# Performance work log

Hardware: AMD Instinct MI355X
Metric: run time of the kernel (lower is better)

## Reference

```python
import jax, jax.numpy as jnp
import numpy as np

N, D, H, E, K = 4096, 512, 2048, 8, 2  # tokens, input/output dim, expert hidden, num_experts, top_k


def setup_inputs() -> dict:
    key = jax.random.key(0)
    k_x, k_r, k_w1, k_b1, k_w2, k_b2 = jax.random.split(key, 6)
    input_batch = jax.random.normal(k_x, (N, D), dtype=jnp.float32)
    # Router-style top-k selection: guarantees the K expert ids per token are distinct
    # (required by the torch nonzero-based dispatch) and probabilities are a softmax
    # over the selected logits, matching a standard MoE sampler.
    router_logits = jax.random.normal(k_r, (N, E), dtype=jnp.float32)
    top_vals, top_idx = jax.lax.top_k(router_logits, K)
    probabilities = jax.nn.softmax(top_vals, axis=-1)            # [N, K]
    indices = top_idx.astype(jnp.int64)                          # [N, K]
    scale = 0.02
    W1 = scale * jax.random.normal(k_w1, (E, D, H), dtype=jnp.float32)
    b1 = jnp.zeros((E, H), dtype=jnp.float32)
    W2 = scale * jax.random.normal(k_w2, (E, H, D), dtype=jnp.float32)
    b2 = jnp.zeros((E, D), dtype=jnp.float32)
    return {"input_batch": input_batch, "probabilities": probabilities, "indices": indices,
            "W1": W1, "b1": b1, "W2": W2, "b2": b2}


def reference(input_batch, probabilities, indices, W1, b1, W2, b2):
    # Each expert is a dense 2-layer GELU MLP. The torch module gathers the tokens
    # assigned to each expert, runs the expert, concatenates, sorts back to original
    # flattened [N*K] order, applies probability weighting AFTER the experts, then
    # reshapes to [N, K, D] and sums over K. That is mathematically:
    #   out[t] = sum_k probabilities[t, k] * expert_{indices[t, k]}(input_batch[t])
    h = jax.nn.gelu(jnp.einsum('nd,edh->enh', input_batch, W1) + b1[:, None, :])  # [E, N, H]
    y = jnp.einsum('enh,ehd->end', h, W2) + b2[:, None, :]                         # [E, N, D]
    y = jnp.transpose(y, (1, 0, 2))                                                # [N, E, D]
    sel = jnp.take_along_axis(y, indices[:, :, None], axis=1)                      # [N, K, D]
    output = jnp.sum(sel * probabilities[:, :, None], axis=1)                      # [N, D]
    total_loss = jnp.float32(0.0)  # no sampler / expert aux losses in this config
    return output, total_loss
```

## Files before the change

### kernel.cpp

```cpp
#include <hip/hip_runtime.h>
#include <cstdint>
#include <cstddef>

#define NTOK 4096
#define DIMD 512
#define HIDH 2048
#define NEXP 8
#define TOPK 2
#define NSLOT (NTOK*TOPK)
#define SLACK 128
#define YROWS (NSLOT+SLACK)

#define BM 128
#define BN 128
#define BK 32

typedef short bf16x8_t __attribute__((ext_vector_type(8)));
typedef float f32x4_t  __attribute__((ext_vector_type(4)));

__device__ __forceinline__ unsigned short f2b(float f){
  unsigned int x = __float_as_uint(f);
  unsigned int r = (x + 0x7FFFu + ((x >> 16) & 1u)) >> 16;
  return (unsigned short)r;
}

__device__ __forceinline__ float gelu_tanh(float x) {
  float z2 = 1.5957691216057308f * fmaf(0.044715f * x, x * x, x);
  return x / (1.f + __expf(-z2));
}

__device__ __forceinline__ void gl_lds16(const void* g, void* l){
  __builtin_amdgcn_global_load_lds((const __attribute__((address_space(1))) void*)g,
                                   (__attribute__((address_space(3))) void*)l, 16, 0, 0);
}


__global__ __launch_bounds__(256) void cvt_x(const float* __restrict__ x, unsigned short* __restrict__ xb){
  int i = blockIdx.x*256 + threadIdx.x;
  if (i >= (NTOK*DIMD)/4) return;
  float4 v = ((const float4*)x)[i];
  ushort4 o; o.x=f2b(v.x); o.y=f2b(v.y); o.z=f2b(v.z); o.w=f2b(v.w);
  ((ushort4*)xb)[i] = o;
}

__global__ __launch_bounds__(256) void transpose_cvt(const float* __restrict__ src,
                                                     unsigned short* __restrict__ dst,
                                                     int R, int C){
  int e = blockIdx.z;
  src += (size_t)e*R*C; dst += (size_t)e*R*C;
  int c0 = blockIdx.x*64, r0 = blockIdx.y*64;
  __shared__ float t[64][65];
  int tr = threadIdx.x >> 4, tc = threadIdx.x & 15;
  #pragma unroll
  for (int i=0;i<4;i++){
    int r = tr + i*16;
    float4 v = *(const float4*)(src + (size_t)(r0 + r)*C + c0 + tc*4);
    t[r][tc*4+0]=v.x; t[r][tc*4+1]=v.y; t[r][tc*4+2]=v.z; t[r][tc*4+3]=v.w;
  }
  __syncthreads();
  #pragma unroll
  for (int i=0;i<4;i++){
    int c = tr + i*16;
    ushort4 o;
    o.x = f2b(t[tc*4+0][c]); o.y = f2b(t[tc*4+1][c]);
    o.z = f2b(t[tc*4+2][c]); o.w = f2b(t[tc*4+3][c]);
    *(ushort4*)(dst + (size_t)(c0 + c)*R + r0 + tc*4) = o;
  }
}


__global__ void count_k(const int* __restrict__ I, int* __restrict__ meta){
  int i = blockIdx.x*256+threadIdx.x;
  if (i < NSLOT) atomicAdd(&meta[I[i]], 1);
}
__global__ void scan_k(int* __restrict__ meta){
  if (threadIdx.x==0 && blockIdx.x==0){
    int s=0;
    for(int e=0;e<NEXP;e++){ meta[16+e]=s; s+=meta[e]; }
  }
}
__global__ void fill_k(const int* __restrict__ I, int* __restrict__ meta,
                       int* __restrict__ tokOf, int* __restrict__ rowOf){
  int i = blockIdx.x*256+threadIdx.x;
  if (i < NSLOT){
    int e = I[i];
    int pos = meta[16+e] + atomicAdd(&meta[8+e], 1);
    tokOf[pos] = i >> 1;
    rowOf[i] = pos;
  }
}


__global__ __launch_bounds__(256,2) void gemm1(
    const unsigned short* __restrict__ Xb, const unsigned short* __restrict__ W1t,
    const float* __restrict__ B1, const int* __restrict__ meta,
    const int* __restrict__ tokOf, unsigned short* __restrict__ H)
{
  const int e = blockIdx.z;
  const int cnt = meta[e];
  const int row0 = blockIdx.y * BM;
  if (row0 >= cnt) return;
  const int off = meta[16+e];
  const int h0 = blockIdx.x * BN;

  __shared__ unsigned short As[3][BM*BK];
  __shared__ unsigned short Bs[3][BN*BK];

  const int tid = threadIdx.x;
  const int ar0 = tid >> 2;
  const int ksw = (((tid & 3) ^ ((tid >> 3) & 3)) << 3);
  int s0 = min(off + row0 + ar0,      NSLOT-1);
  int s1 = min(off + row0 + ar0 + 64, NSLOT-1);
  const unsigned short* srcA0 = Xb + (size_t)tokOf[s0]*DIMD + ksw;
  const unsigned short* srcA1 = Xb + (size_t)tokOf[s1]*DIMD + ksw;
  const unsigned short* srcB0 = W1t + ((size_t)e*HIDH + h0 + ar0)*DIMD + ksw;
  const unsigned short* srcB1 = srcB0 + (size_t)64*DIMD;

  const int lane = tid & 63;
  const int wid  = tid >> 6;
  const int wr = (wid >> 1) * 64, wc = (wid & 1) * 64;
  const int l15 = lane & 15, kg = lane >> 4;

  int offA[4], offB[4];
  #pragma unroll
  for (int m=0;m<4;m++){
    int r  = wr + m*16 + l15;
    int rb = wc + m*16 + l15;
    offA[m] = r *BK + ((kg ^ ((r >>1)&3)) << 3);
    offB[m] = rb*BK + ((kg ^ ((rb>>1)&3)) << 3);
  }

  f32x4_t acc[4][4];
  #pragma unroll
  for (int i=0;i<4;i++){
    #pragma unroll
    for (int j=0;j<4;j++) acc[i][j] = (f32x4_t){0.f,0.f,0.f,0.f};
  }

  auto stage = [&](int buf, int kt){
    const int k0 = kt * BK;
    gl_lds16(srcA0 + k0, &As[buf][tid*8]);
    gl_lds16(srcA1 + k0, &As[buf][2048 + tid*8]);
    gl_lds16(srcB0 + k0, &Bs[buf][tid*8]);
    gl_lds16(srcB1 + k0, &Bs[buf][2048 + tid*8]);
  };

  auto compute = [&](int buf){
    bf16x8_t af[4], bfr[4];
    #pragma unroll
    for (int m=0;m<4;m++) af[m]  = *(const bf16x8_t*)&As[buf][offA[m]];
    #pragma unroll
    for (int n=0;n<4;n++) bfr[n] = *(const bf16x8_t*)&Bs[buf][offB[n]];
    #pragma unroll
    for (int m=0;m<4;m++){
      #pragma unroll
      for (int n=0;n<4;n++)
        acc[m][n] = __builtin_amdgcn_mfma_f32_16x16x32_bf16(af[m], bfr[n], acc[m][n], 0,0,0);
    }
  };

  constexpr int NS = DIMD/BK;
  stage(0,0); stage(1,1); stage(2,2);
  for (int t = 0; t + 4 <= NS; ++t){
    asm volatile("s_waitcnt vmcnt(8)" ::: "memory");
    __builtin_amdgcn_s_barrier();
    compute(t%3);
    __builtin_amdgcn_s_barrier();
    stage(t%3, t+3);
  }
  asm volatile("s_waitcnt vmcnt(8)" ::: "memory");
  __builtin_amdgcn_s_barrier();
  compute((NS-3)%3);
  asm volatile("s_waitcnt vmcnt(4)" ::: "memory");
  __builtin_amdgcn_s_barrier();
  compute((NS-2)%3);
  asm volatile("s_waitcnt vmcnt(0)" ::: "memory");
  __builtin_amdgcn_s_barrier();
  compute((NS-1)%3);

  const int r4 = (lane >> 4) * 4;
  #pragma unroll
  for (int n=0;n<4;n++){
    int hc = h0 + wc + n*16 + l15;
    float b1v = B1[(size_t)e*HIDH + hc];
    #pragma unroll
    for (int m=0;m<4;m++){
      int rbase = row0 + wr + m*16 + r4;
      #pragma unroll
      for (int r=0;r<4;r++){
        int row = rbase + r;
        if (row < cnt){
          float v = gelu_tanh(acc[m][n][r] + b1v);
          H[(size_t)(off + row)*HIDH + hc] = f2b(v);
        }
      }
    }
  }
}


__global__ __launch_bounds__(256,2) void gemm2(
    const unsigned short* __restrict__ H, const unsigned short* __restrict__ W2t,
    const int* __restrict__ meta, float* __restrict__ Y, int nsplit)
{
  const int e = blockIdx.z;
  const int cnt = meta[e];
  const int row0 = blockIdx.y * BM;
  if (row0 >= cnt) return;
  const int off = meta[16+e];
  const int ncol = DIMD/BN;
  const int d0 = (blockIdx.x % ncol) * BN;
  const int kc = blockIdx.x / ncol;
  const int kchunk = HIDH / nsplit;
  const int kbase = kc * kchunk;

  __shared__ unsigned short As[3][BM*BK];
  __shared__ unsigned short Bs[3][BN*BK];

  const int tid = threadIdx.x;
  const int ar0 = tid >> 2;
  const int ksw = (((tid & 3) ^ ((tid >> 3) & 3)) << 3);
  const unsigned short* srcA0 = H + (size_t)(off + row0 + ar0)*HIDH + kbase + ksw;
  const unsigned short* srcA1 = srcA0 + (size_t)64*HIDH;
  const unsigned short* srcB0 = W2t + ((size_t)e*DIMD + d0 + ar0)*HIDH + kbase + ksw;
  const unsigned short* srcB1 = srcB0 + (size_t)64*HIDH;

  const int lane = tid & 63;
  const int wid  = tid >> 6;
  const int wr = (wid >> 1) * 64, wc = (wid & 1) * 64;
  const int l15 = lane & 15, kg = lane >> 4;

  int offA[4], offB[4];
  #pragma unroll
  for (int m=0;m<4;m++){
    int r  = wr + m*16 + l15;
    int rb = wc + m*16 + l15;
    offA[m] = r *BK + ((kg ^ ((r >>1)&3)) << 3);
    offB[m] = rb*BK + ((kg ^ ((rb>>1)&3)) << 3);
  }

  f32x4_t acc[4][4];
  #pragma unroll
  for (int i=0;i<4;i++){
    #pragma unroll
    for (int j=0;j<4;j++) acc[i][j] = (f32x4_t){0.f,0.f,0.f,0.f};
  }

  auto stage = [&](int buf, int kt){
    const int k0 = kt * BK;
    gl_lds16(srcA0 + k0, &As[buf][tid*8]);
    gl_lds16(srcA1 + k0, &As[buf][2048 + tid*8]);
    gl_lds16(srcB0 + k0, &Bs[buf][tid*8]);
    gl_lds16(srcB1 + k0, &Bs[buf][2048 + tid*8]);
  };

  auto compute = [&](int buf){
    bf16x8_t af[4], bfr[4];
    #pragma unroll
    for (int m=0;m<4;m++) af[m]  = *(const bf16x8_t*)&As[buf][offA[m]];
    #pragma unroll
    for (int n=0;n<4;n++) bfr[n] = *(const bf16x8_t*)&Bs[buf][offB[n]];
    #pragma unroll
    for (int m=0;m<4;m++){
      #pragma unroll
      for (int n=0;n<4;n++)
        acc[m][n] = __builtin_amdgcn_mfma_f32_16x16x32_bf16(af[m], bfr[n], acc[m][n], 0,0,0);
    }
  };

  const int NS = kchunk / BK;
  stage(0,0); stage(1,1); stage(2,2);
  for (int t = 0; t + 4 <= NS; ++t){
    asm volatile("s_waitcnt vmcnt(8)" ::: "memory");
    __builtin_amdgcn_s_barrier();
    compute(t%3);
    __builtin_amdgcn_s_barrier();
    stage(t%3, t+3);
  }
  asm volatile("s_waitcnt vmcnt(8)" ::: "memory");
  __builtin_amdgcn_s_barrier();
  compute((NS-3)%3);
  asm volatile("s_waitcnt vmcnt(4)" ::: "memory");
  __builtin_amdgcn_s_barrier();
  compute((NS-2)%3);
  asm volatile("s_waitcnt vmcnt(0)" ::: "memory");
  __builtin_amdgcn_s_barrier();
  compute((NS-1)%3);

  float* Yp = Y + (size_t)kc * YROWS * DIMD;
  const int r4 = (lane >> 4) * 4;
  #pragma unroll
  for (int m=0;m<4;m++){
    int rbase = row0 + wr + m*16 + r4;
    #pragma unroll
    for (int r=0;r<4;r++){
      int row = rbase + r;
      if (row < cnt){
        float* yp = Yp + (size_t)(off + row)*DIMD + d0 + wc + l15;
        #pragma unroll
        for (int n=0;n<4;n++) yp[n*16] = acc[m][n][r];
      }
    }
  }
}


__global__ __launch_bounds__(128) void reduce_k(
    const float* __restrict__ P, const int* __restrict__ I, const int* __restrict__ rowOf,
    const float* __restrict__ Y, const float* __restrict__ B2, float* __restrict__ out,
    int nsplit)
{
  int t = blockIdx.x; int d4 = threadIdx.x;
  float4 a = make_float4(0.f,0.f,0.f,0.f);
  #pragma unroll
  for (int k=0;k<TOPK;k++){
    int i = t*TOPK + k;
    float p = P[i]; int e = I[i]; int r = rowOf[i];
    float4 b = *(const float4*)(B2 + (size_t)e*DIMD + d4*4);
    float4 y = make_float4(b.x, b.y, b.z, b.w);
    for (int c=0;c<nsplit;c++){
      float4 v = *(const float4*)(Y + (size_t)c*YROWS*DIMD + (size_t)r*DIMD + d4*4);
      y.x += v.x; y.y += v.y; y.z += v.z; y.w += v.w;
    }
    a.x = fmaf(p, y.x, a.x); a.y = fmaf(p, y.y, a.y);
    a.z = fmaf(p, y.z, a.z); a.w = fmaf(p, y.w, a.w);
  }
  *(float4*)(out + (size_t)t*DIMD + d4*4) = a;
}


#define CAP (NTOK*TOPK)
#define ROWS 32
#define HC 64
#define NTHR 256
#define XS_LD 516
#define HS_LD 36

__global__ void fb_build(const int* __restrict__ idx, const float* __restrict__ probs,
                         int* __restrict__ counts, int* __restrict__ tok,
                         float* __restrict__ pr) {
    int i = blockIdx.x * blockDim.x + threadIdx.x;
    if (i >= NTOK * TOPK) return;
    int t = i / TOPK;
    int e = idx[i];
    float p = probs[i];
    int pos = atomicAdd(&counts[e], 1);
    tok[e * CAP + pos] = t;
    pr[e * CAP + pos] = p;
}

__global__ __launch_bounds__(NTHR)
void fb_moe(const float* __restrict__ X,
            const float* __restrict__ W1, const float* __restrict__ B1,
            const float* __restrict__ W2, const float* __restrict__ B2,
            const int* __restrict__ counts, const int* __restrict__ tok,
            const float* __restrict__ pr, float* __restrict__ out)
{
    const int e = blockIdx.y;
    const int cnt = counts[e];
    const int r0 = blockIdx.x * ROWS;
    if (r0 >= cnt) return;
    const int nr = min(ROWS, cnt - r0);

    extern __shared__ float smem[];
    float* Xs = smem;
    float* Hs = smem + ROWS * XS_LD;
    const int tid = threadIdx.x;

    for (int i = tid; i < ROWS * (DIMD / 4); i += NTHR) {
        int r = i >> 7;
        int c4 = i & 127;
        float4 v = make_float4(0.f, 0.f, 0.f, 0.f);
        if (r < nr) {
            int t = tok[e * CAP + r0 + r];
            v = *(const float4*)(X + (size_t)t * DIMD + c4 * 4);
        }
        *(float4*)(Xs + r * XS_LD + c4 * 4) = v;
    }
    __syncthreads();

    const int hq = tid & 15;
    const int rp = tid >> 4;
    const int wv = tid >> 6;
    const int ln = tid & 63;

    float yacc[8][8];
    #pragma unroll
    for (int r = 0; r < 8; ++r){
        #pragma unroll
        for (int c = 0; c < 8; ++c) yacc[r][c] = 0.f;
    }

    const float* w1base = W1 + (size_t)e * DIMD * HIDH;
    const float* w2base = W2 + (size_t)e * HIDH * DIMD;
    const float* b1base = B1 + e * HIDH;

    for (int h0 = 0; h0 < HIDH; h0 += HC) {
        float acc0[4] = {0.f, 0.f, 0.f, 0.f};
        float acc1[4] = {0.f, 0.f, 0.f, 0.f};
        const float* w1p = w1base + h0 + hq * 4;
        const float* xr0 = Xs + (rp * 2) * XS_LD;
        const float* xr1 = xr0 + XS_LD;
        #pragma unroll 2
        for (int d = 0; d < DIMD; d += 4) {
            float4 xa = *(const float4*)(xr0 + d);
            float4 xb = *(const float4*)(xr1 + d);
            float4 w0 = *(const float4*)(w1p + (size_t)(d + 0) * HIDH);
            float4 w1v = *(const float4*)(w1p + (size_t)(d + 1) * HIDH);
            float4 w2v = *(const float4*)(w1p + (size_t)(d + 2) * HIDH);
            float4 w3v = *(const float4*)(w1p + (size_t)(d + 3) * HIDH);
            float xav[4] = {xa.x, xa.y, xa.z, xa.w};
            float xbv[4] = {xb.x, xb.y, xb.z, xb.w};
            float4 wsv[4] = {w0, w1v, w2v, w3v};
            #pragma unroll
            for (int dd = 0; dd < 4; ++dd) {
                acc0[0] = fmaf(xav[dd], wsv[dd].x, acc0[0]);
                acc0[1] = fmaf(xav[dd], wsv[dd].y, acc0[1]);
                acc0[2] = fmaf(xav[dd], wsv[dd].z, acc0[2]);
                acc0[3] = fmaf(xav[dd], wsv[dd].w, acc0[3]);
                acc1[0] = fmaf(xbv[dd], wsv[dd].x, acc1[0]);
                acc1[1] = fmaf(xbv[dd], wsv[dd].y, acc1[1]);
                acc1[2] = fmaf(xbv[dd], wsv[dd].z, acc1[2]);
                acc1[3] = fmaf(xbv[dd], wsv[dd].w, acc1[3]);
            }
        }
        {
            float4 b1v = *(const float4*)(b1base + h0 + hq * 4);
            float bb[4] = {b1v.x, b1v.y, b1v.z, b1v.w};
            #pragma unroll
            for (int j = 0; j < 4; ++j) {
                Hs[(hq * 4 + j) * HS_LD + rp * 2]     = gelu_tanh(acc0[j] + bb[j]);
                Hs[(hq * 4 + j) * HS_LD + rp * 2 + 1] = gelu_tanh(acc1[j] + bb[j]);
            }
        }
        __syncthreads();

        const float* w2p = w2base + (size_t)h0 * DIMD;
        #pragma unroll 4
        for (int hc = 0; hc < HC; ++hc) {
            float4 wA = *(const float4*)(w2p + (size_t)hc * DIMD + ln * 4);
            float4 wB = *(const float4*)(w2p + (size_t)hc * DIMD + 256 + ln * 4);
            float4 hv0 = *(const float4*)(Hs + hc * HS_LD + wv * 8);
            float4 hv1 = *(const float4*)(Hs + hc * HS_LD + wv * 8 + 4);
            float hr[8] = {hv0.x, hv0.y, hv0.z, hv0.w, hv1.x, hv1.y, hv1.z, hv1.w};
            #pragma unroll
            for (int r = 0; r < 8; ++r) {
                yacc[r][0] = fmaf(hr[r], wA.x, yacc[r][0]);
                yacc[r][1] = fmaf(hr[r], wA.y, yacc[r][1]);
                yacc[r][2] = fmaf(hr[r], wA.z, yacc[r][2]);
                yacc[r][3] = fmaf(hr[r], wA.w, yacc[r][3]);
                yacc[r][4] = fmaf(hr[r], wB.x, yacc[r][4]);
                yacc[r][5] = fmaf(hr[r], wB.y, yacc[r][5]);
                yacc[r][6] = fmaf(hr[r], wB.z, yacc[r][6]);
                yacc[r][7] = fmaf(hr[r], wB.w, yacc[r][7]);
            }
        }
        __syncthreads();
    }

    const float* b2p = B2 + e * DIMD;
    float4 b2A = *(const float4*)(b2p + ln * 4);
    float4 b2B = *(const float4*)(b2p + 256 + ln * 4);
    float bA[4] = {b2A.x, b2A.y, b2A.z, b2A.w};
    float bB[4] = {b2B.x, b2B.y, b2B.z, b2B.w};
    #pragma unroll
    for (int r = 0; r < 8; ++r) {
        int rg = wv * 8 + r;
        if (rg < nr) {
            int t = tok[e * CAP + r0 + rg];
            float p = pr[e * CAP + r0 + rg];
            float* op = out + (size_t)t * DIMD;
            #pragma unroll
            for (int j = 0; j < 4; ++j) {
                atomicAdd(op + ln * 4 + j,        p * (yacc[r][j] + bA[j]));
                atomicAdd(op + 256 + ln * 4 + j,  p * (yacc[r][4 + j] + bB[j]));
            }
        }
    }
}


extern "C" void kernel_launch(void* const* d_in, const int* in_sizes, int n_in,
                              void* d_out, int out_size, void* d_ws, size_t ws_size,
                              hipStream_t stream) {
    const float* X  = (const float*)d_in[0];
    const float* P  = (const float*)d_in[1];
    const int*   I  = (const int*)d_in[2];
    const float* W1 = (const float*)d_in[3];
    const float* B1 = (const float*)d_in[4];
    const float* W2 = (const float*)d_in[5];
    const float* B2 = (const float*)d_in[6];
    float* out = (float*)d_out;
    char* ws = (char*)d_ws;

    int nsplit = 0;
    size_t o_meta=0, o_tok=0, o_row=0, o_xb=0, o_w1t=0, o_w2t=0, o_h=0, o_y=0;
    const int cand[3] = {4, 2, 1};
    for (int ci = 0; ci < 3; ++ci) {
        int ns = cand[ci];
        size_t cur = 0;
        auto alloc = [&](size_t b){ size_t p = cur; cur += (b + 255) & ~(size_t)255; return p; };
        size_t m_ = alloc(256);
        size_t t_ = alloc((size_t)NSLOT*4);
        size_t r_ = alloc((size_t)NSLOT*4);
        size_t x_ = alloc((size_t)NTOK*DIMD*2);
        size_t w1_ = alloc((size_t)NEXP*DIMD*HIDH*2);
        size_t w2_ = alloc((size_t)NEXP*DIMD*HIDH*2);
        size_t h_ = alloc((size_t)YROWS*HIDH*2);
        size_t y_ = alloc((size_t)ns*YROWS*DIMD*4);
        if (cur <= ws_size) {
            nsplit = ns;
            o_meta=m_; o_tok=t_; o_row=r_; o_xb=x_; o_w1t=w1_; o_w2t=w2_; o_h=h_; o_y=y_;
            break;
        }
    }

    if (nsplit > 0) {
        int* meta = (int*)(ws + o_meta);
        int* tokOf = (int*)(ws + o_tok);
        int* rowOf = (int*)(ws + o_row);
        unsigned short* Xb  = (unsigned short*)(ws + o_xb);
        unsigned short* W1t = (unsigned short*)(ws + o_w1t);
        unsigned short* W2t = (unsigned short*)(ws + o_w2t);
        unsigned short* Hb  = (unsigned short*)(ws + o_h);
        float* Yb = (float*)(ws + o_y);

        hipMemsetAsync(meta, 0, 256, stream);
        cvt_x<<<(NTOK*DIMD/4 + 255)/256, 256, 0, stream>>>(X, Xb);
        transpose_cvt<<<dim3(HIDH/64, DIMD/64, NEXP), 256, 0, stream>>>(W1, W1t, DIMD, HIDH);
        transpose_cvt<<<dim3(DIMD/64, HIDH/64, NEXP), 256, 0, stream>>>(W2, W2t, HIDH, DIMD);
        count_k<<<NSLOT/256, 256, 0, stream>>>(I, meta);
        scan_k<<<1, 64, 0, stream>>>(meta);
        fill_k<<<NSLOT/256, 256, 0, stream>>>(I, meta, tokOf, rowOf);
        gemm1<<<dim3(HIDH/BN, NTOK/BM, NEXP), 256, 0, stream>>>(Xb, W1t, B1, meta, tokOf, Hb);
        gemm2<<<dim3((DIMD/BN)*nsplit, NTOK/BM, NEXP), 256, 0, stream>>>(Hb, W2t, meta, Yb, nsplit);
        reduce_k<<<NTOK, 128, 0, stream>>>(P, I, rowOf, Yb, B2, out, nsplit);
    } else {
        int*   counts = (int*)ws;
        int*   tok    = (int*)(ws + 64);
        float* pr     = (float*)(ws + 64 + (size_t)NEXP * CAP * sizeof(int));

        hipMemsetAsync(counts, 0, NEXP * sizeof(int), stream);
        hipMemsetAsync(d_out, 0, (size_t)out_size * sizeof(float), stream);
        fb_build<<<(NTOK * TOPK + 255) / 256, 256, 0, stream>>>(I, P, counts, tok, pr);
        size_t smem = (size_t)(ROWS * XS_LD + HC * HS_LD) * sizeof(float);
        hipFuncSetAttribute((const void*)fb_moe,
                            hipFuncAttributeMaxDynamicSharedMemorySize, (int)smem);
        fb_moe<<<dim3(CAP / ROWS, NEXP), NTHR, smem, stream>>>(
            X, W1, B1, W2, B2, counts, tok, pr, out);
    }
}
```

Measured before the change: 198.4 us.

## Fuse MoE combine into gemm2 via atomics and persistent row-block loops

Removes the split-K partial Y buffer and the separate reduce kernel: gemm2 now weights each expert-row result by its routing probability, adds bias on the first K chunk, and atomically accumulates straight into the zeroed output. Both GEMMs switch from a 3D grid with early exits on empty row blocks to a 1D grid where each block strides over row blocks (step 8), with expert as the fastest-varying index. This cuts the Y write/read traffic and one launch, at the cost of float atomics into the output (nondeterministic summation order, contention) and an extra output memset.

```diff
diff --git a/kernel.cpp b/kernel.cpp
--- a/kernel.cpp
+++ b/kernel.cpp
@@ -8,8 +8,6 @@
 #define NEXP 8
 #define TOPK 2
 #define NSLOT (NTOK*TOPK)
-#define SLACK 128
-#define YROWS (NSLOT+SLACK)
 
 #define BM 128
 #define BN 128
@@ -79,16 +77,18 @@
     for(int e=0;e<NEXP;e++){ meta[16+e]=s; s+=meta[e]; }
   }
 }
-__global__ void fill_k(const int* __restrict__ I, int* __restrict__ meta,
-                       int* __restrict__ tokOf, int* __restrict__ rowOf){
+__global__ void fill_k(const int* __restrict__ I, const float* __restrict__ P,
+                       int* __restrict__ meta, int* __restrict__ tokOf,
+                       float* __restrict__ pOf){
   int i = blockIdx.x*256+threadIdx.x;
   if (i < NSLOT){
     int e = I[i];
     int pos = meta[16+e] + atomicAdd(&meta[8+e], 1);
     tokOf[pos] = i >> 1;
-    rowOf[i] = pos;
-  }
-}
+    pOf[pos] = P[i];
+  }
+}
+
 
 
 __global__ __launch_bounds__(256,2) void gemm1(
@@ -96,23 +96,22 @@
     const float* __restrict__ B1, const int* __restrict__ meta,
     const int* __restrict__ tokOf, unsigned short* __restrict__ H)
 {
-  const int e = blockIdx.z;
+  const int bid = blockIdx.x;
+  const int e   = bid & 7;
+  const int rst = bid >> 3;
+  const int hb  = rst & 15;
+  const int rb0 = rst >> 4;
   const int cnt = meta[e];
-  const int row0 = blockIdx.y * BM;
-  if (row0 >= cnt) return;
   const int off = meta[16+e];
-  const int h0 = blockIdx.x * BN;
+  const int h0 = hb * BN;
 
   __shared__ unsigned short As[3][BM*BK];
-  __shared__ unsigned short Bs[3][BN*BK];
+  __shared__ unsigned short Bs[3][BM*BK];
 
   const int tid = threadIdx.x;
   const int ar0 = tid >> 2;
   const int ksw = (((tid & 3) ^ ((tid >> 3) & 3)) << 3);
-  int s0 = min(off + row0 + ar0,      NSLOT-1);
-  int s1 = min(off + row0 + ar0 + 64, NSLOT-1);
-  const unsigned short* srcA0 = Xb + (size_t)tokOf[s0]*DIMD + ksw;
-  const unsigned short* srcA1 = Xb + (size_t)tokOf[s1]*DIMD + ksw;
+
   const unsigned short* srcB0 = W1t + ((size_t)e*HIDH + h0 + ar0)*DIMD + ksw;
   const unsigned short* srcB1 = srcB0 + (size_t)64*DIMD;
 
@@ -125,103 +124,110 @@
   #pragma unroll
   for (int m=0;m<4;m++){
     int r  = wr + m*16 + l15;
-    int rb = wc + m*16 + l15;
-    offA[m] = r *BK + ((kg ^ ((r >>1)&3)) << 3);
-    offB[m] = rb*BK + ((kg ^ ((rb>>1)&3)) << 3);
-  }
-
-  f32x4_t acc[4][4];
-  #pragma unroll
-  for (int i=0;i<4;i++){
+    int rbn = wc + m*16 + l15;
+    offA[m] = r  *BK + ((kg ^ ((r  >>1)&3)) << 3);
+    offB[m] = rbn*BK + ((kg ^ ((rbn>>1)&3)) << 3);
+  }
+
+  for (int rb = rb0; rb * BM < cnt; rb += 8) {
+    const int row0 = rb * BM;
+    const int s0 = min(off + row0 + ar0,      NSLOT-1);
+    const int s1 = min(off + row0 + ar0 + 64, NSLOT-1);
+    const unsigned short* srcA0 = Xb + (size_t)tokOf[s0]*DIMD + ksw;
+    const unsigned short* srcA1 = Xb + (size_t)tokOf[s1]*DIMD + ksw;
+
+    f32x4_t acc[4][4];
     #pragma unroll
-    for (int j=0;j<4;j++) acc[i][j] = (f32x4_t){0.f,0.f,0.f,0.f};
-  }
-
-  auto stage = [&](int buf, int kt){
-    const int k0 = kt * BK;
-    gl_lds16(srcA0 + k0, &As[buf][tid*8]);
-    gl_lds16(srcA1 + k0, &As[buf][2048 + tid*8]);
-    gl_lds16(srcB0 + k0, &Bs[buf][tid*8]);
-    gl_lds16(srcB1 + k0, &Bs[buf][2048 + tid*8]);
-  };
-
-  auto compute = [&](int buf){
-    bf16x8_t af[4], bfr[4];
-    #pragma unroll
-    for (int m=0;m<4;m++) af[m]  = *(const bf16x8_t*)&As[buf][offA[m]];
-    #pragma unroll
-    for (int n=0;n<4;n++) bfr[n] = *(const bf16x8_t*)&Bs[buf][offB[n]];
-    #pragma unroll
-    for (int m=0;m<4;m++){
-      #pragma unroll
-      for (int n=0;n<4;n++)
-        acc[m][n] = __builtin_amdgcn_mfma_f32_16x16x32_bf16(af[m], bfr[n], acc[m][n], 0,0,0);
-    }
-  };
-
-  constexpr int NS = DIMD/BK;
-  stage(0,0); stage(1,1); stage(2,2);
-  for (int t = 0; t + 4 <= NS; ++t){
+    for (int i=0;i<4;i++){
+      #pragma unroll
+      for (int j=0;j<4;j++) acc[i][j] = (f32x4_t){0.f,0.f,0.f,0.f};
+    }
+
+    auto stage = [&](int buf, int kt){
+      const int k0 = kt * BK;
+      gl_lds16(srcA0 + k0, &As[buf][tid*8]);
+      gl_lds16(srcA1 + k0, &As[buf][2048 + tid*8]);
+      gl_lds16(srcB0 + k0, &Bs[buf][tid*8]);
+      gl_lds16(srcB1 + k0, &Bs[buf][2048 + tid*8]);
+    };
+
+    auto compute = [&](int buf){
+      bf16x8_t af[4], bfr[4];
+      #pragma unroll
+      for (int m=0;m<4;m++) af[m]  = *(const bf16x8_t*)&As[buf][offA[m]];
+      #pragma unroll
+      for (int n=0;n<4;n++) bfr[n] = *(const bf16x8_t*)&Bs[buf][offB[n]];
+      #pragma unroll
+      for (int m=0;m<4;m++){
+        #pragma unroll
+        for (int n=0;n<4;n++)
+          acc[m][n] = __builtin_amdgcn_mfma_f32_16x16x32_bf16(af[m], bfr[n], acc[m][n], 0,0,0);
+      }
+    };
+
+    constexpr int NS = DIMD/BK;
+    stage(0,0); stage(1,1); stage(2,2);
+    for (int t = 0; t + 4 <= NS; ++t){
+      asm volatile("s_waitcnt vmcnt(8)" ::: "memory");
+      __builtin_amdgcn_s_barrier();
+      compute(t%3);
+      __builtin_amdgcn_s_barrier();
+      stage(t%3, t+3);
+    }
     asm volatile("s_waitcnt vmcnt(8)" ::: "memory");
     __builtin_amdgcn_s_barrier();
-    compute(t%3);
+    compute((NS-3)%3);
+    asm volatile("s_waitcnt vmcnt(4)" ::: "memory");
     __builtin_amdgcn_s_barrier();
-    stage(t%3, t+3);
-  }
-  asm volatile("s_waitcnt vmcnt(8)" ::: "memory");
-  __builtin_amdgcn_s_barrier();
-  compute((NS-3)%3);
-  asm volatile("s_waitcnt vmcnt(4)" ::: "memory");
-  __builtin_amdgcn_s_barrier();
-  compute((NS-2)%3);
-  asm volatile("s_waitcnt vmcnt(0)" ::: "memory");
-  __builtin_amdgcn_s_barrier();
-  compute((NS-1)%3);
-
-  const int r4 = (lane >> 4) * 4;
-  #pragma unroll
-  for (int n=0;n<4;n++){
-    int hc = h0 + wc + n*16 + l15;
-    float b1v = B1[(size_t)e*HIDH + hc];
+    compute((NS-2)%3);
+    asm volatile("s_waitcnt vmcnt(0)" ::: "memory");
+    __builtin_amdgcn_s_barrier();
+    compute((NS-1)%3);
+
+    const int r4 = kg * 4;
     #pragma unroll
-    for (int m=0;m<4;m++){
-      int rbase = row0 + wr + m*16 + r4;
-      #pragma unroll
-      for (int r=0;r<4;r++){
-        int row = rbase + r;
-        if (row < cnt){
-          float v = gelu_tanh(acc[m][n][r] + b1v);
-          H[(size_t)(off + row)*HIDH + hc] = f2b(v);
+    for (int n=0;n<4;n++){
+      int hc = h0 + wc + n*16 + l15;
+      float b1v = B1[(size_t)e*HIDH + hc];
+      #pragma unroll
+      for (int m=0;m<4;m++){
+        int rbase = row0 + wr + m*16 + r4;
+        #pragma unroll
+        for (int r=0;r<4;r++){
+          int row = rbase + r;
+          if (row < cnt)
+            H[(size_t)(off + row)*HIDH + hc] = f2b(gelu_tanh(acc[m][n][r] + b1v));
         }
       }
     }
+    __syncthreads();
   }
 }
 
 
 __global__ __launch_bounds__(256,2) void gemm2(
-    const unsigned short* __restrict__ H, const unsigned short* __restrict__ W2t,
-    const int* __restrict__ meta, float* __restrict__ Y, int nsplit)
+    const unsigned short* __restrict__ Hb, const unsigned short* __restrict__ W2t,
+    const float* __restrict__ B2, const int* __restrict__ meta,
+    const int* __restrict__ tokOf, const float* __restrict__ pOf,
+    float* __restrict__ out)
 {
-  const int e = blockIdx.z;
+  const int bid = blockIdx.x;
+  const int e   = bid & 7;
+  const int rst = bid >> 3;
+  const int d0  = (rst & 3) * BN;
+  const int kc  = (rst >> 2) & 3;
+  const int rb0 = rst >> 4;
   const int cnt = meta[e];
-  const int row0 = blockIdx.y * BM;
-  if (row0 >= cnt) return;
   const int off = meta[16+e];
-  const int ncol = DIMD/BN;
-  const int d0 = (blockIdx.x % ncol) * BN;
-  const int kc = blockIdx.x / ncol;
-  const int kchunk = HIDH / nsplit;
-  const int kbase = kc * kchunk;
+  const int kbase = kc * (HIDH/4);
 
   __shared__ unsigned short As[3][BM*BK];
-  __shared__ unsigned short Bs[3][BN*BK];
+  __shared__ unsigned short Bs[3][BM*BK];
 
   const int tid = threadIdx.x;
   const int ar0 = tid >> 2;
   const int ksw = (((tid & 3) ^ ((tid >> 3) & 3)) << 3);
-  const unsigned short* srcA0 = H + (size_t)(off + row0 + ar0)*HIDH + kbase + ksw;
-  const unsigned short* srcA1 = srcA0 + (size_t)64*HIDH;
+
   const unsigned short* srcB0 = W2t + ((size_t)e*DIMD + d0 + ar0)*HIDH + kbase + ksw;
   const unsigned short* srcB1 = srcB0 + (size_t)64*HIDH;
 
@@ -234,98 +240,89 @@
   #pragma unroll
   for (int m=0;m<4;m++){
     int r  = wr + m*16 + l15;
-    int rb = wc + m*16 + l15;
-    offA[m] = r *BK + ((kg ^ ((r >>1)&3)) << 3);
-    offB[m] = rb*BK + ((kg ^ ((rb>>1)&3)) << 3);
-  }
-
-  f32x4_t acc[4][4];
-  #pragma unroll
-  for (int i=0;i<4;i++){
+    int rbn = wc + m*16 + l15;
+    offA[m] = r  *BK + ((kg ^ ((r  >>1)&3)) << 3);
+    offB[m] = rbn*BK + ((kg ^ ((rbn>>1)&3)) << 3);
+  }
+
+  for (int rb = rb0; rb * BM < cnt; rb += 8) {
+    const int row0 = rb * BM;
+    const int s0 = min(off + row0 + ar0,      NSLOT-1);
+    const int s1 = min(off + row0 + ar0 + 64, NSLOT-1);
+    const unsigned short* srcA0 = Hb + (size_t)s0*HIDH + kbase + ksw;
+    const unsigned short* srcA1 = Hb + (size_t)s1*HIDH + kbase + ksw;
+
+    f32x4_t acc[4][4];
     #pragma unroll
-    for (int j=0;j<4;j++) acc[i][j] = (f32x4_t){0.f,0.f,0.f,0.f};
-  }
-
-  auto stage = [&](int buf, int kt){
-    const int k0 = kt * BK;
-    gl_lds16(srcA0 + k0, &As[buf][tid*8]);
-    gl_lds16(srcA1 + k0, &As[buf][2048 + tid*8]);
-    gl_lds16(srcB0 + k0, &Bs[buf][tid*8]);
-    gl_lds16(srcB1 + k0, &Bs[buf][2048 + tid*8]);
-  };
-
-  auto compute = [&](int buf){
-    bf16x8_t af[4], bfr[4];
-    #pragma unroll
-    for (int m=0;m<4;m++) af[m]  = *(const bf16x8_t*)&As[buf][offA[m]];
-    #pragma unroll
-    for (int n=0;n<4;n++) bfr[n] = *(const bf16x8_t*)&Bs[buf][offB[n]];
+    for (int i=0;i<4;i++){
+      #pragma unroll
+      for (int j=0;j<4;j++) acc[i][j] = (f32x4_t){0.f,0.f,0.f,0.f};
+    }
+
+    auto stage = [&](int buf, int kt){
+      const int k0 = kt * BK;
+      gl_lds16(srcA0 + k0, &As[buf][tid*8]);
+      gl_lds16(srcA1 + k0, &As[buf][2048 + tid*8]);
+      gl_lds16(srcB0 + k0, &Bs[buf][tid*8]);
+      gl_lds16(srcB1 + k0, &Bs[buf][2048 + tid*8]);
+    };
+
+    auto compute = [&](int buf){
+      bf16x8_t af[4], bfr[4];
+      #pragma unroll
+      for (int m=0;m<4;m++) af[m]  = *(const bf16x8_t*)&As[buf][offA[m]];
+      #pragma unroll
+      for (int n=0;n<4;n++) bfr[n] = *(const bf16x8_t*)&Bs[buf][offB[n]];
+      #pragma unroll
+      for (int m=0;m<4;m++){
+        #pragma unroll
+        for (int n=0;n<4;n++)
+          acc[m][n] = __builtin_amdgcn_mfma_f32_16x16x32_bf16(af[m], bfr[n], acc[m][n], 0,0,0);
+      }
+    };
+
+    constexpr int NS = (HIDH/4)/BK;
+    stage(0,0); stage(1,1); stage(2,2);
+    for (int t = 0; t + 4 <= NS; ++t){
+      asm volatile("s_waitcnt vmcnt(8)" ::: "memory");
+      __builtin_amdgcn_s_barrier();
+      compute(t%3);
+      __builtin_amdgcn_s_barrier();
+      stage(t%3, t+3);
+    }
+    asm volatile("s_waitcnt vmcnt(8)" ::: "memory");
+    __builtin_amdgcn_s_barrier();
+    compute((NS-3)%3);
+    asm volatile("s_waitcnt vmcnt(4)" ::: "memory");
+    __builtin_amdgcn_s_barrier();
+    compute((NS-2)%3);
+    asm volatile("s_waitcnt vmcnt(0)" ::: "memory");
+    __builtin_amdgcn_s_barrier();
+    compute((NS-1)%3);
+
+    const int r4 = kg * 4;
     #pragma unroll
     for (int m=0;m<4;m++){
-      #pragma unroll
-      for (int n=0;n<4;n++)
-        acc[m][n] = __builtin_amdgcn_mfma_f32_16x16x32_bf16(af[m], bfr[n], acc[m][n], 0,0,0);
-    }
-  };
-
-  const int NS = kchunk / BK;
-  stage(0,0); stage(1,1); stage(2,2);
-  for (int t = 0; t + 4 <= NS; ++t){
-    asm volatile("s_waitcnt vmcnt(8)" ::: "memory");
-    __builtin_amdgcn_s_barrier();
-    compute(t%3);
-    __builtin_amdgcn_s_barrier();
-    stage(t%3, t+3);
-  }
-  asm volatile("s_waitcnt vmcnt(8)" ::: "memory");
-  __builtin_amdgcn_s_barrier();
-  compute((NS-3)%3);
-  asm volatile("s_waitcnt vmcnt(4)" ::: "memory");
-  __builtin_amdgcn_s_barrier();
-  compute((NS-2)%3);
-  asm volatile("s_waitcnt vmcnt(0)" ::: "memory");
-  __builtin_amdgcn_s_barrier();
-  compute((NS-1)%3);
-
-  float* Yp = Y + (size_t)kc * YROWS * DIMD;
-  const int r4 = (lane >> 4) * 4;
-  #pragma unroll
-  for (int m=0;m<4;m++){
-    int rbase = row0 + wr + m*16 + r4;
-    #pragma unroll
-    for (int r=0;r<4;r++){
-      int row = rbase + r;
-      if (row < cnt){
-        float* yp = Yp + (size_t)(off + row)*DIMD + d0 + wc + l15;
-        #pragma unroll
-        for (int n=0;n<4;n++) yp[n*16] = acc[m][n][r];
+      int rbase = row0 + wr + m*16 + r4;
+      #pragma unroll
+      for (int r=0;r<4;r++){
+        int row = rbase + r;
+        if (row < cnt){
+          const int slot = off + row;
+          const int t = tokOf[slot];
+          const float p = pOf[slot];
+          float* op = out + (size_t)t*DIMD + d0 + wc + l15;
+          #pragma unroll
+          for (int n=0;n<4;n++){
+            float v = acc[m][n][r];
+            if (kc == 0) v += B2[(size_t)e*DIMD + d0 + wc + n*16 + l15];
+            atomicAdd(op + n*16, p * v);
+          }
+        }
       }
     }
-  }
-}
-
-
-__global__ __launch_bounds__(128) void reduce_k(
-    const float* __restrict__ P, const int* __restrict__ I, const int* __restrict__ rowOf,
-    const float* __restrict__ Y, const float* __restrict__ B2, float* __restrict__ out,
-    int nsplit)
-{
-  int t = blockIdx.x; int d4 = threadIdx.x;
-  float4 a = make_float4(0.f,0.f,0.f,0.f);
-  #pragma unroll
-  for (int k=0;k<TOPK;k++){
-    int i = t*TOPK + k;
-    float p = P[i]; int e = I[i]; int r = rowOf[i];
-    float4 b = *(const float4*)(B2 + (size_t)e*DIMD + d4*4);
-    float4 y = make_float4(b.x, b.y, b.z, b.w);
-    for (int c=0;c<nsplit;c++){
-      float4 v = *(const float4*)(Y + (size_t)c*YROWS*DIMD + (size_t)r*DIMD + d4*4);
-      y.x += v.x; y.y += v.y; y.z += v.z; y.w += v.w;
-    }
-    a.x = fmaf(p, y.x, a.x); a.y = fmaf(p, y.y, a.y);
-    a.z = fmaf(p, y.z, a.z); a.w = fmaf(p, y.w, a.w);
-  }
-  *(float4*)(out + (size_t)t*DIMD + d4*4) = a;
+    __syncthreads();
+  }
 }
 
 
@@ -493,48 +490,37 @@
     float* out = (float*)d_out;
     char* ws = (char*)d_ws;
 
-    int nsplit = 0;
-    size_t o_meta=0, o_tok=0, o_row=0, o_xb=0, o_w1t=0, o_w2t=0, o_h=0, o_y=0;
-    const int cand[3] = {4, 2, 1};
-    for (int ci = 0; ci < 3; ++ci) {
-        int ns = cand[ci];
-        size_t cur = 0;
-        auto alloc = [&](size_t b){ size_t p = cur; cur += (b + 255) & ~(size_t)255; return p; };
-        size_t m_ = alloc(256);
-        size_t t_ = alloc((size_t)NSLOT*4);
-        size_t r_ = alloc((size_t)NSLOT*4);
-        size_t x_ = alloc((size_t)NTOK*DIMD*2);
-        size_t w1_ = alloc((size_t)NEXP*DIMD*HIDH*2);
-        size_t w2_ = alloc((size_t)NEXP*DIMD*HIDH*2);
-        size_t h_ = alloc((size_t)YROWS*HIDH*2);
-        size_t y_ = alloc((size_t)ns*YROWS*DIMD*4);
-        if (cur <= ws_size) {
-            nsplit = ns;
-            o_meta=m_; o_tok=t_; o_row=r_; o_xb=x_; o_w1t=w1_; o_w2t=w2_; o_h=h_; o_y=y_;
-            break;
-        }
-    }
-
-    if (nsplit > 0) {
+    size_t cur = 0;
+    auto alloc = [&](size_t b){ size_t p = cur; cur += (b + 255) & ~(size_t)255; return p; };
+    size_t o_meta = alloc(256);
+    size_t o_tok  = alloc((size_t)NSLOT*4);
+    size_t o_p    = alloc((size_t)NSLOT*4);
+    size_t o_xb   = alloc((size_t)NTOK*DIMD*2);
+    size_t o_w1t  = alloc((size_t)NEXP*DIMD*HIDH*2);
+    size_t o_w2t  = alloc((size_t)NEXP*DIMD*HIDH*2);
+    size_t o_h    = alloc((size_t)NSLOT*HIDH*2);
+    size_t need = cur;
+
+    if (ws_size >= need) {
         int* meta = (int*)(ws + o_meta);
         int* tokOf = (int*)(ws + o_tok);
-        int* rowOf = (int*)(ws + o_row);
+        float* pOf = (float*)(ws + o_p);
         unsigned short* Xb  = (unsigned short*)(ws + o_xb);
         unsigned short* W1t = (unsigned short*)(ws + o_w1t);
         unsigned short* W2t = (unsigned short*)(ws + o_w2t);
         unsigned short* Hb  = (unsigned short*)(ws + o_h);
-        float* Yb = (float*)(ws + o_y);
 
         hipMemsetAsync(meta, 0, 256, stream);
+        hipMemsetAsync(d_out, 0, (size_t)out_size * sizeof(float), stream);
         cvt_x<<<(NTOK*DIMD/4 + 255)/256, 256, 0, stream>>>(X, Xb);
         transpose_cvt<<<dim3(HIDH/64, DIMD/64, NEXP), 256, 0, stream>>>(W1, W1t, DIMD, HIDH);
         transpose_cvt<<<dim3(DIMD/64, HIDH/64, NEXP), 256, 0, stream>>>(W2, W2t, HIDH, DIMD);
         count_k<<<NSLOT/256, 256, 0, stream>>>(I, meta);
         scan_k<<<1, 64, 0, stream>>>(meta);
-        fill_k<<<NSLOT/256, 256, 0, stream>>>(I, meta, tokOf, rowOf);
-        gemm1<<<dim3(HIDH/BN, NTOK/BM, NEXP), 256, 0, stream>>>(Xb, W1t, B1, meta, tokOf, Hb);
-        gemm2<<<dim3((DIMD/BN)*nsplit, NTOK/BM, NEXP), 256, 0, stream>>>(Hb, W2t, meta, Yb, nsplit);
-        reduce_k<<<NTOK, 128, 0, stream>>>(P, I, rowOf, Yb, B2, out, nsplit);
+        fill_k<<<NSLOT/256, 256, 0, stream>>>(I, P, meta, tokOf, pOf);
+
+        gemm1<<<16*8*NEXP, 256, 0, stream>>>(Xb, W1t, B1, meta, tokOf, Hb);
+        gemm2<<<4*4*8*NEXP, 256, 0, stream>>>(Hb, W2t, B2, meta, tokOf, pOf, out);
     } else {
         int*   counts = (int*)ws;
         int*   tok    = (int*)(ws + 64);
```

Measured after the change: 252.5 us. 27.3% more time.
